# Kernel optimization log

Hardware: AMD Instinct MI355X
Metric: run time of the kernel (lower is better)

## Reference

```python
import jax, jax.numpy as jnp
import numpy as np

PERIOD = 15          # hardcoded in the torch module's forward: STL(series, 15)
N_SEASONAL = 7       # statsmodels STL default seasonal smoother length
N_TREND = 29         # smallest odd >= 1.5*p/(1-1.5/7) = 28.64 -> 29 (statsmodels default)
N_LOWPASS = 17       # smallest odd > period (statsmodels default)
N_INNER = 2          # statsmodels: robust=False -> 2 inner iterations, 0 outer


def _loess_matrix(n, q, ts):
    """Dense linear operator for degree-1 LOESS smoothing of a length-n series
    evaluated at (possibly out-of-range) integer positions ts. Non-robust LOESS is
    linear in y, so smoothing == matmul with this constant matrix."""
    M = np.zeros((len(ts), n), dtype=np.float64)
    qq = min(q, n)
    for i, t in enumerate(ts):
        left = int(np.clip(t - (q - 1) // 2, 0, n - qq))
        right = left + qq - 1
        h = max(t - left, right - t)
        if q > n:
            h += (q - n) / 2.0
        xs = np.arange(left, right + 1, dtype=np.float64)
        w = np.clip(1.0 - (np.abs(xs - t) / h) ** 3, 0.0, None) ** 3  # tricube
        w = w / w.sum()
        xbar = (w * xs).sum()
        var = (w * (xs - xbar) ** 2).sum()
        a = w.copy()
        if var > 1e-12:  # degree-1 local linear fit; fall back to deg-0 if degenerate
            a = w * (1.0 + (t - xbar) * (xs - xbar) / var)
        M[i, left:right + 1] = a
    return M.astype(np.float32)


def _ma(x, k):
    """Moving average of window k along last axis (valid mode)."""
    cs = jnp.cumsum(x, axis=-1)
    cs = jnp.concatenate([jnp.zeros(x.shape[:-1] + (1,), x.dtype), cs], axis=-1)
    return (cs[..., k:] - cs[..., :-k]) / k


def setup_inputs() -> dict:
    key = jax.random.key(0)
    x = jax.random.normal(key, (128, 480, 256), dtype=jnp.float32)  # [B, T, C]
    return {"x": x}


def reference(x):
    B, T, Cc = x.shape
    p = PERIOD
    n_sub = T // p  # cycle-subseries length; T chosen divisible by period

    # Constant LOESS smoothing operators (numpy, baked in as jit constants)
    M_seas = jnp.asarray(_loess_matrix(n_sub, N_SEASONAL, np.arange(-1, n_sub + 1)))  # (n_sub+2, n_sub)
    M_lp = jnp.asarray(_loess_matrix(T, N_LOWPASS, np.arange(T)))                     # (T, T)
    M_trend = jnp.asarray(_loess_matrix(T, N_TREND, np.arange(T)))                    # (T, T)

    y = jnp.transpose(x, (0, 2, 1))  # [B, C, T]
    trend = jnp.zeros_like(y)
    seasonal = jnp.zeros_like(y)

    for _ in range(N_INNER):  # STL inner loop (Cleveland 1990, non-robust)
        # 1. detrend
        D = y - trend
        # 2. cycle-subseries LOESS smoothing, extended one period each side
        Dsub = D.reshape(B, Cc, n_sub, p)                      # subseries along axis 2
        Cext = jnp.einsum('sn,bcnp->bcsp', M_seas, Dsub)       # [B,C,n_sub+2,p]
        Cext = Cext.reshape(B, Cc, (n_sub + 2) * p)            # time order, length T+2p
        # 3. low-pass: MA(p) x2, MA(3), then LOESS(n_l)
        lp = _ma(_ma(_ma(Cext, p), p), 3)                      # length T
        L = jnp.einsum('tn,bcn->bct', M_lp, lp)
        # 4. seasonal = smoothed subseries (center T) minus low-pass
        seasonal = Cext[..., p:p + T] - L
        # 5+6. deseasonalize and trend LOESS
        trend = jnp.einsum('tn,bcn->bct', M_trend, y - seasonal)

    resid = y - seasonal - trend
    seas_plus_resid = jnp.transpose(seasonal + resid, (0, 2, 1))  # [B, T, C]
    trend_out = jnp.transpose(trend, (0, 2, 1))
    return (seas_plus_resid, trend_out)
```

## Files before the change

kernel.cpp:

```cpp
#include <hip/hip_runtime.h>
#include <hip/hip_bf16.h>
#include <stdint.h>

#define TLEN 480
#define NB 128
#define NC 256

typedef short bf16x8 __attribute__((ext_vector_type(8)));
typedef float f32x4 __attribute__((ext_vector_type(4)));
typedef unsigned short u16;
typedef unsigned int u32;

__device__ inline u16 f2bf(float f) {
    union { float f; uint32_t u; } v; v.f = f;
    uint32_t u = v.u;
    return (u16)((u + 0x7fffu + ((u >> 16) & 1u)) >> 16);
}

__device__ inline u32 pack2bf(float lo, float hi) {
    return __builtin_amdgcn_perm(__float_as_uint(hi), __float_as_uint(lo), 0x07060302u);
}

__device__ int loess_w(int t, int n, int q, float* out) {
    int left = t - (q - 1) / 2;
    if (left < 0) left = 0;
    if (left > n - q) left = n - q;
    int right = left + q - 1;
    int h = (t - left) > (right - t) ? (t - left) : (right - t);
    double w[29];
    double wsum = 0.0;
    for (int i = 0; i < q; ++i) {
        double dist = fabs((double)(left + i - t)) / (double)h;
        double u = 1.0 - dist * dist * dist;
        if (u < 0.0) u = 0.0;
        double wv = u * u * u;
        w[i] = wv; wsum += wv;
    }
    for (int i = 0; i < q; ++i) w[i] /= wsum;
    double xbar = 0.0;
    for (int i = 0; i < q; ++i) xbar += w[i] * (double)(left + i);
    double var = 0.0;
    for (int i = 0; i < q; ++i) { double d = (double)(left + i) - xbar; var += w[i] * d * d; }
    if (var > 1e-12) {
        double tb = (double)t - xbar;
        for (int i = 0; i < q; ++i) {
            double d = (double)(left + i) - xbar;
            out[i] = (float)(w[i] * (1.0 + tb * d / var));
        }
    } else {
        for (int i = 0; i < q; ++i) out[i] = (float)w[i];
    }
    return left;
}

__global__ void k_loess(float* Ms, float* w3, float* MlpC, float* MtC) {
    int gid = blockIdx.x * 256 + threadIdx.x;
    if (gid < 34) {
        float wl[7];
        int left = loess_w(gid - 1, 32, 7, wl);
        float* row = Ms + gid * 32;
        #pragma unroll
        for (int i = 0; i < 32; ++i) row[i] = 0.0f;
        for (int i = 0; i < 7; ++i) row[left + i] = wl[i];
    } else if (gid < 514) {
        int t = gid - 34;
        float wl[17];
        loess_w(t, TLEN, 17, wl);
        for (int i = 0; i < 17; ++i) MlpC[t * 17 + i] = wl[i];
    } else if (gid < 994) {
        int t = gid - 514;
        float wl[29];
        loess_w(t, TLEN, 29, wl);
        for (int i = 0; i < 29; ++i) MtC[t * 29 + i] = wl[i];
    } else if (gid < 1025) {
        int d = gid - 994;
        int cnt = 0;
        for (int c = 0; c < 3; ++c)
            for (int a = 0; a < 15; ++a) {
                int b = d - a - c;
                if (b >= 0 && b < 15) cnt++;
            }
        w3[d] = (float)((double)cnt / 675.0);
    }
}

__global__ void k_S(const float* __restrict__ Ms, const float* __restrict__ w3,
                    const float* __restrict__ MlpC, float* __restrict__ S) {
    int id = blockIdx.x * 256 + threadIdx.x;
    if (id >= TLEN * TLEN) return;
    int t = id / TLEN, u = id - t * TLEN;
    int nu = u / 15, ju = u - nu * 15;
    int slp = t - 8;
    if (slp < 0) slp = 0;
    if (slp > TLEN - 17) slp = TLEN - 17;
    float acc = 0.0f;
    for (int k = 0; k < 17; ++k) {
        int i = slp + k;
        int s_lo = (i - ju + 14) / 15;
        float g = 0.0f;
        #pragma unroll
        for (int ds = 0; ds < 3; ++ds) {
            int s = s_lo + ds;
            int d = s * 15 + ju - i;
            if (s >= 0 && s < 34 && d >= 0 && d <= 30)
                g += Ms[s * 32 + nu] * w3[d];
        }
        acc += MlpC[t * 17 + k] * g;
    }
    float val = -acc;
    if (t % 15 == ju) val += Ms[(1 + t / 15) * 32 + nu];
    S[id] = val;
}

__global__ void k_VU(const float* __restrict__ MtC, const float* __restrict__ S,
                     float* __restrict__ U, float* __restrict__ V) {
    int id = blockIdx.x * 256 + threadIdx.x;
    if (id >= TLEN * TLEN) return;
    int t = id / TLEN, u = id - t * TLEN;
    int st = t - 14;
    if (st < 0) st = 0;
    if (st > TLEN - 29) st = TLEN - 29;
    float acc = 0.0f;
    for (int k = 0; k < 29; ++k)
        acc += MtC[t * 29 + k] * S[(size_t)(st + k) * TLEN + u];
    float mt = (u >= st && u < st + 29) ? MtC[t * 29 + (u - st)] : 0.0f;
    V[id] = acc;
    U[id] = mt - acc;
}

__global__ void k_A(const float* __restrict__ U, const float* __restrict__ V,
                    u16* __restrict__ Abf) {
    __shared__ float Vs[16][17];
    __shared__ float Us[16][17];
    int tx = threadIdx.x, ty = threadIdx.y;
    int u = blockIdx.x * 16 + tx;
    int t = blockIdx.y * 16 + ty;
    float acc = 0.0f;
    for (int kt = 0; kt < 30; ++kt) {
        Vs[ty][tx] = V[(size_t)t * TLEN + kt * 16 + tx];
        Us[ty][tx] = U[(size_t)(kt * 16 + ty) * TLEN + u];
        __syncthreads();
        #pragma unroll
        for (int e = 0; e < 16; ++e) acc += Vs[ty][e] * Us[e][tx];
        __syncthreads();
    }
    Abf[(size_t)t * TLEN + u] = f2bf(U[(size_t)t * TLEN + u] + acc);
}

__global__ __launch_bounds__(256, 2)
void k_gemm(const u16* __restrict__ A, const float* __restrict__ x,
            float* __restrict__ out0, float* __restrict__ out1) {
    __shared__ u16 Xs[64 * 488];
    int b = blockIdx.x;
    int t0 = blockIdx.y * 96;
    int cz = blockIdx.z * 64;
    int tid = threadIdx.x;
    int wave = tid >> 6, lane = tid & 63;
    int lane15 = lane & 15, quad = lane >> 4;
    int wm = wave & 1, wn = wave >> 1;

    int wq  = tid & 15;
    int kkq = tid >> 4;
    const float* xp0 = x + (size_t)b * TLEN * NC + (size_t)(kkq * 4) * NC + cz + wq * 4;
    u32* l32 = (u32*)Xs;
    int lbase = (wq * 4) * 244 + kkq * 2;

    float4 ra[4], rb[4];
    {
        #pragma unroll
        for (int q = 0; q < 4; ++q) ra[q] = *(const float4*)(xp0 + q * NC);
    }
    #pragma unroll
    for (int p = 0; p < 8; ++p) {
        float4* cur = (p & 1) ? rb : ra;
        float4* nxt = (p & 1) ? ra : rb;
        if (p < 7) {
            if (p + 1 < 7 || kkq < 8) {
                const float* xp = xp0 + (size_t)(p + 1) * 64 * NC;
                #pragma unroll
                for (int q = 0; q < 4; ++q) nxt[q] = *(const float4*)(xp + q * NC);
            }
        }
        if (p < 7 || kkq < 8) {
            const float* fl = (const float*)cur;
            int o = lbase + p * 32;
            #pragma unroll
            for (int cc = 0; cc < 4; ++cc) {
                uint2 w;
                w.x = pack2bf(fl[0 * 4 + cc], fl[1 * 4 + cc]);
                w.y = pack2bf(fl[2 * 4 + cc], fl[3 * 4 + cc]);
                *(uint2*)(l32 + o + cc * 244) = w;
            }
        }
    }
    __syncthreads();

    const u16* bp0 = A + (size_t)(t0 + wn * 48 + lane15) * TLEN + quad * 8;
    int arow = (wm * 32 + lane15) * 488 + quad * 8;

    f32x4 acc[2][3] = {};
    bf16x8 bcur[3], bnxt[3], acur[2], anxt[2];
    #pragma unroll
    for (int j = 0; j < 3; ++j) bcur[j] = *(const bf16x8*)(bp0 + (size_t)j * 16 * TLEN);
    acur[0] = *(const bf16x8*)&Xs[arow];
    acur[1] = *(const bf16x8*)&Xs[arow + 16 * 488];

    #pragma unroll
    for (int s = 0; s < 15; ++s) {
        bf16x8* bc = (s & 1) ? bnxt : bcur;
        bf16x8* bn = (s & 1) ? bcur : bnxt;
        bf16x8* ac = (s & 1) ? anxt : acur;
        bf16x8* an = (s & 1) ? acur : anxt;
        if (s < 14) {
            int k = (s + 1) * 32;
            #pragma unroll
            for (int j = 0; j < 3; ++j)
                bn[j] = *(const bf16x8*)(bp0 + (size_t)j * 16 * TLEN + k);
            an[0] = *(const bf16x8*)&Xs[arow + k];
            an[1] = *(const bf16x8*)&Xs[arow + 16 * 488 + k];
        }
        #pragma unroll
        for (int j = 0; j < 3; ++j) {
            acc[0][j] = __builtin_amdgcn_mfma_f32_16x16x32_bf16(ac[0], bc[j], acc[0][j], 0, 0, 0);
            acc[1][j] = __builtin_amdgcn_mfma_f32_16x16x32_bf16(ac[1], bc[j], acc[1][j], 0, 0, 0);
        }
    }

    __syncthreads();

    float* T = (float*)Xs;
    float* R = T + 96 * 68;
    #pragma unroll
    for (int j = 0; j < 3; ++j) {
        int tl = wn * 48 + j * 16 + lane15;
        #pragma unroll
        for (int i = 0; i < 2; ++i) {
            int clb = wm * 32 + i * 16 + quad * 4;
            f32x4 tv = acc[i][j];
            size_t gb = ((size_t)b * TLEN + t0 + tl) * NC + cz + clb;
            f32x4 xv = *(const f32x4*)(x + gb);
            *(f32x4*)&T[tl * 68 + clb] = tv;
            *(f32x4*)&R[tl * 68 + clb] = xv - tv;
        }
    }
    __syncthreads();

    #pragma unroll
    for (int v = 0; v < 6; ++v) {
        int id = v * 256 + tid;
        int tl = id >> 4, c4 = (id & 15) * 4;
        size_t gb = ((size_t)b * TLEN + t0 + tl) * NC + cz + c4;
        f32x4 tv = *(const f32x4*)&T[tl * 68 + c4];
        f32x4 rv = *(const f32x4*)&R[tl * 68 + c4];
        __builtin_nontemporal_store(tv, (f32x4*)(out1 + gb));
        __builtin_nontemporal_store(rv, (f32x4*)(out0 + gb));
    }
}

extern "C" void kernel_launch(void* const* d_in, const int* in_sizes, int n_in,
                              void* d_out, int out_size, void* d_ws, size_t ws_size,
                              hipStream_t stream) {
    const float* x = (const float*)d_in[0];
    float* out0 = (float*)d_out;
    float* out1 = (float*)d_out + (size_t)NB * TLEN * NC;

    char* ws = (char*)d_ws;
    size_t oMs  = 0;
    size_t oW3  = oMs + 4352;
    size_t oLpC = oW3 + 128;
    size_t oMtC = oLpC + 32640;
    size_t oS   = oMtC + 55680;
    size_t oU   = oS + 921600;
    size_t oV   = oU + 921600;
    size_t oA   = oV + 921600;

    float* Ms   = (float*)(ws + oMs);
    float* w3   = (float*)(ws + oW3);
    float* MlpC = (float*)(ws + oLpC);
    float* MtC  = (float*)(ws + oMtC);
    float* S    = (float*)(ws + oS);
    float* U    = (float*)(ws + oU);
    float* V    = (float*)(ws + oV);
    u16*   Abf  = (u16*)(ws + oA);

    k_loess<<<5, 256, 0, stream>>>(Ms, w3, MlpC, MtC);
    k_S<<<900, 256, 0, stream>>>(Ms, w3, MlpC, S);
    k_VU<<<900, 256, 0, stream>>>(MtC, S, U, V);
    k_A<<<dim3(30, 30), dim3(16, 16), 0, stream>>>(U, V, Abf);
    k_gemm<<<dim3(NB, 5, 4), 256, 0, stream>>>(Abf, x, out0, out1);
}
```

Before: 254.0 us.

## Halve GEMM channel tile to 32 and raise occupancy; template LOESS weight helper

```diff
diff --git a/kernel.cpp b/kernel.cpp
--- a/kernel.cpp
+++ b/kernel.cpp
@@ -21,34 +21,41 @@
     return __builtin_amdgcn_perm(__float_as_uint(hi), __float_as_uint(lo), 0x07060302u);
 }
 
-__device__ int loess_w(int t, int n, int q, float* out) {
-    int left = t - (q - 1) / 2;
+template<int N, int Q>
+__device__ __forceinline__ int loess_wT(int t, float* out) {
+    int left = t - (Q - 1) / 2;
     if (left < 0) left = 0;
-    if (left > n - q) left = n - q;
-    int right = left + q - 1;
+    if (left > N - Q) left = N - Q;
+    int right = left + Q - 1;
     int h = (t - left) > (right - t) ? (t - left) : (right - t);
-    double w[29];
+    double w[Q];
     double wsum = 0.0;
-    for (int i = 0; i < q; ++i) {
+    #pragma unroll
+    for (int i = 0; i < Q; ++i) {
         double dist = fabs((double)(left + i - t)) / (double)h;
         double u = 1.0 - dist * dist * dist;
         if (u < 0.0) u = 0.0;
         double wv = u * u * u;
         w[i] = wv; wsum += wv;
     }
-    for (int i = 0; i < q; ++i) w[i] /= wsum;
+    #pragma unroll
+    for (int i = 0; i < Q; ++i) w[i] /= wsum;
     double xbar = 0.0;
-    for (int i = 0; i < q; ++i) xbar += w[i] * (double)(left + i);
+    #pragma unroll
+    for (int i = 0; i < Q; ++i) xbar += w[i] * (double)(left + i);
     double var = 0.0;
-    for (int i = 0; i < q; ++i) { double d = (double)(left + i) - xbar; var += w[i] * d * d; }
+    #pragma unroll
+    for (int i = 0; i < Q; ++i) { double d = (double)(left + i) - xbar; var += w[i] * d * d; }
     if (var > 1e-12) {
         double tb = (double)t - xbar;
-        for (int i = 0; i < q; ++i) {
+        #pragma unroll
+        for (int i = 0; i < Q; ++i) {
             double d = (double)(left + i) - xbar;
             out[i] = (float)(w[i] * (1.0 + tb * d / var));
         }
     } else {
-        for (int i = 0; i < q; ++i) out[i] = (float)w[i];
+        #pragma unroll
+        for (int i = 0; i < Q; ++i) out[i] = (float)w[i];
     }
     return left;
 }
@@ -57,20 +64,23 @@
     int gid = blockIdx.x * 256 + threadIdx.x;
     if (gid < 34) {
         float wl[7];
-        int left = loess_w(gid - 1, 32, 7, wl);
+        int left = loess_wT<32, 7>(gid - 1, wl);
         float* row = Ms + gid * 32;
         #pragma unroll
         for (int i = 0; i < 32; ++i) row[i] = 0.0f;
+        #pragma unroll
         for (int i = 0; i < 7; ++i) row[left + i] = wl[i];
     } else if (gid < 514) {
         int t = gid - 34;
         float wl[17];
-        loess_w(t, TLEN, 17, wl);
+        loess_wT<TLEN, 17>(t, wl);
+        #pragma unroll
         for (int i = 0; i < 17; ++i) MlpC[t * 17 + i] = wl[i];
     } else if (gid < 994) {
         int t = gid - 514;
         float wl[29];
-        loess_w(t, TLEN, 29, wl);
+        loess_wT<TLEN, 29>(t, wl);
+        #pragma unroll
         for (int i = 0; i < 29; ++i) MtC[t * 29 + i] = wl[i];
     } else if (gid < 1025) {
         int d = gid - 994;
@@ -147,23 +157,23 @@
     Abf[(size_t)t * TLEN + u] = f2bf(U[(size_t)t * TLEN + u] + acc);
 }
 
-__global__ __launch_bounds__(256, 2)
+__global__ __launch_bounds__(256, 5)
 void k_gemm(const u16* __restrict__ A, const float* __restrict__ x,
             float* __restrict__ out0, float* __restrict__ out1) {
-    __shared__ u16 Xs[64 * 488];
+    __shared__ u16 Xs[32 * 488];
     int b = blockIdx.x;
     int t0 = blockIdx.y * 96;
-    int cz = blockIdx.z * 64;
+    int cz = blockIdx.z * 32;
     int tid = threadIdx.x;
     int wave = tid >> 6, lane = tid & 63;
     int lane15 = lane & 15, quad = lane >> 4;
-    int wm = wave & 1, wn = wave >> 1;
-
-    int wq  = tid & 15;
-    int kkq = tid >> 4;
-    const float* xp0 = x + (size_t)b * TLEN * NC + (size_t)(kkq * 4) * NC + cz + wq * 4;
+    int wt = wave & 1, wc = wave >> 1;
+
+    int cq  = tid & 7;
+    int kq0 = tid >> 3;
+    const float* xp0 = x + (size_t)b * TLEN * NC + (size_t)(kq0 * 4) * NC + cz + cq * 4;
     u32* l32 = (u32*)Xs;
-    int lbase = (wq * 4) * 244 + kkq * 2;
+    int lbase = (cq * 4) * 244 + kq0 * 2;
 
     float4 ra[4], rb[4];
     {
@@ -171,19 +181,19 @@
         for (int q = 0; q < 4; ++q) ra[q] = *(const float4*)(xp0 + q * NC);
     }
     #pragma unroll
-    for (int p = 0; p < 8; ++p) {
+    for (int p = 0; p < 4; ++p) {
         float4* cur = (p & 1) ? rb : ra;
         float4* nxt = (p & 1) ? ra : rb;
-        if (p < 7) {
-            if (p + 1 < 7 || kkq < 8) {
-                const float* xp = xp0 + (size_t)(p + 1) * 64 * NC;
+        if (p < 3) {
+            if (p + 1 < 3 || kq0 < 24) {
+                const float* xp = xp0 + (size_t)(p + 1) * 128 * NC;
                 #pragma unroll
                 for (int q = 0; q < 4; ++q) nxt[q] = *(const float4*)(xp + q * NC);
             }
         }
-        if (p < 7 || kkq < 8) {
+        if (p < 3 || kq0 < 24) {
             const float* fl = (const float*)cur;
-            int o = lbase + p * 32;
+            int o = lbase + p * 64;
             #pragma unroll
             for (int cc = 0; cc < 4; ++cc) {
                 uint2 w;
@@ -195,63 +205,56 @@
     }
     __syncthreads();
 
-    const u16* bp0 = A + (size_t)(t0 + wn * 48 + lane15) * TLEN + quad * 8;
-    int arow = (wm * 32 + lane15) * 488 + quad * 8;
-
-    f32x4 acc[2][3] = {};
-    bf16x8 bcur[3], bnxt[3], acur[2], anxt[2];
+    const u16* bp0 = A + (size_t)(t0 + wt * 48 + lane15) * TLEN + quad * 8;
+    int arow = (wc * 16 + lane15) * 488 + quad * 8;
+
+    f32x4 acc[3] = {};
+    bf16x8 bcur[3], bnxt[3], acur, anxt;
     #pragma unroll
     for (int j = 0; j < 3; ++j) bcur[j] = *(const bf16x8*)(bp0 + (size_t)j * 16 * TLEN);
-    acur[0] = *(const bf16x8*)&Xs[arow];
-    acur[1] = *(const bf16x8*)&Xs[arow + 16 * 488];
+    acur = *(const bf16x8*)&Xs[arow];
 
     #pragma unroll
     for (int s = 0; s < 15; ++s) {
         bf16x8* bc = (s & 1) ? bnxt : bcur;
         bf16x8* bn = (s & 1) ? bcur : bnxt;
-        bf16x8* ac = (s & 1) ? anxt : acur;
-        bf16x8* an = (s & 1) ? acur : anxt;
+        bf16x8& ac = (s & 1) ? anxt : acur;
+        bf16x8& an = (s & 1) ? acur : anxt;
         if (s < 14) {
             int k = (s + 1) * 32;
             #pragma unroll
             for (int j = 0; j < 3; ++j)
                 bn[j] = *(const bf16x8*)(bp0 + (size_t)j * 16 * TLEN + k);
-            an[0] = *(const bf16x8*)&Xs[arow + k];
-            an[1] = *(const bf16x8*)&Xs[arow + 16 * 488 + k];
-        }
-        #pragma unroll
-        for (int j = 0; j < 3; ++j) {
-            acc[0][j] = __builtin_amdgcn_mfma_f32_16x16x32_bf16(ac[0], bc[j], acc[0][j], 0, 0, 0);
-            acc[1][j] = __builtin_amdgcn_mfma_f32_16x16x32_bf16(ac[1], bc[j], acc[1][j], 0, 0, 0);
-        }
+            an = *(const bf16x8*)&Xs[arow + k];
+        }
+        #pragma unroll
+        for (int j = 0; j < 3; ++j)
+            acc[j] = __builtin_amdgcn_mfma_f32_16x16x32_bf16(ac, bc[j], acc[j], 0, 0, 0);
     }
 
     __syncthreads();
 
     float* T = (float*)Xs;
-    float* R = T + 96 * 68;
+    float* R = T + 96 * 36;
     #pragma unroll
     for (int j = 0; j < 3; ++j) {
-        int tl = wn * 48 + j * 16 + lane15;
-        #pragma unroll
-        for (int i = 0; i < 2; ++i) {
-            int clb = wm * 32 + i * 16 + quad * 4;
-            f32x4 tv = acc[i][j];
-            size_t gb = ((size_t)b * TLEN + t0 + tl) * NC + cz + clb;
-            f32x4 xv = *(const f32x4*)(x + gb);
-            *(f32x4*)&T[tl * 68 + clb] = tv;
-            *(f32x4*)&R[tl * 68 + clb] = xv - tv;
-        }
+        int tl = wt * 48 + j * 16 + lane15;
+        int clb = wc * 16 + quad * 4;
+        f32x4 tv = acc[j];
+        size_t gb = ((size_t)b * TLEN + t0 + tl) * NC + cz + clb;
+        f32x4 xv = *(const f32x4*)(x + gb);
+        *(f32x4*)&T[tl * 36 + clb] = tv;
+        *(f32x4*)&R[tl * 36 + clb] = xv - tv;
     }
     __syncthreads();
 
     #pragma unroll
-    for (int v = 0; v < 6; ++v) {
+    for (int v = 0; v < 3; ++v) {
         int id = v * 256 + tid;
-        int tl = id >> 4, c4 = (id & 15) * 4;
+        int tl = id >> 3, c4 = (id & 7) * 4;
         size_t gb = ((size_t)b * TLEN + t0 + tl) * NC + cz + c4;
-        f32x4 tv = *(const f32x4*)&T[tl * 68 + c4];
-        f32x4 rv = *(const f32x4*)&R[tl * 68 + c4];
+        f32x4 tv = *(const f32x4*)&T[tl * 36 + c4];
+        f32x4 rv = *(const f32x4*)&R[tl * 36 + c4];
         __builtin_nontemporal_store(tv, (f32x4*)(out1 + gb));
         __builtin_nontemporal_store(rv, (f32x4*)(out0 + gb));
     }
@@ -287,5 +290,5 @@
     k_S<<<900, 256, 0, stream>>>(Ms, w3, MlpC, S);
     k_VU<<<900, 256, 0, stream>>>(MtC, S, U, V);
     k_A<<<dim3(30, 30), dim3(16, 16), 0, stream>>>(U, V, Abf);
-    k_gemm<<<dim3(NB, 5, 4), 256, 0, stream>>>(Abf, x, out0, out1);
-}
+    k_gemm<<<dim3(NB, 5, 8), 256, 0, stream>>>(Abf, x, out0, out1);
+}
```

Measured after the change: 278.8 us. 9.8% more time.
